# Performance work log

Hardware: AMD Instinct MI355X
Metric: run time of the kernel (lower is better)

Reference implementation:

```python
import jax, jax.numpy as jnp
import numpy as np

DIM = 1024
NUM_HEADS = 16
HEAD_DIM = DIM // NUM_HEADS
SCALE = HEAD_DIM ** -0.5


def setup_inputs() -> dict:
    key = jax.random.key(0)
    ks = jax.random.split(key, 5)
    x = jax.random.normal(ks[0], (8, 1024, DIM), dtype=jnp.float32)
    # nn.Linear default init ~ U(-1/sqrt(fan_in), 1/sqrt(fan_in)); use scaled normals
    w_qkv = jax.random.normal(ks[1], (DIM, 3 * DIM), dtype=jnp.float32) * (DIM ** -0.5)
    b_qkv = jax.random.normal(ks[2], (3 * DIM,), dtype=jnp.float32) * 0.02
    w_proj = jax.random.normal(ks[3], (DIM, DIM), dtype=jnp.float32) * (DIM ** -0.5)
    b_proj = jax.random.normal(ks[4], (DIM,), dtype=jnp.float32) * 0.02
    return {"x": x, "w_qkv": w_qkv, "b_qkv": b_qkv, "w_proj": w_proj, "b_proj": b_proj}


def reference(x, w_qkv, b_qkv, w_proj, b_proj):
    B, N, D = x.shape
    qkv = x @ w_qkv + b_qkv                       # [B, N, 3D]
    qkv = qkv.reshape(B, N, 3, NUM_HEADS, HEAD_DIM)
    qkv = jnp.transpose(qkv, (2, 0, 3, 1, 4))     # [3, B, H, N, hd]
    q, k, v = qkv[0], qkv[1], qkv[2]
    attn = jnp.einsum('bhqd,bhkd->bhqk', q, k) * SCALE
    attn = jax.nn.softmax(attn, axis=-1)
    out = jnp.einsum('bhqk,bhkd->bhqd', attn, v)  # [B, H, N, hd]
    out = jnp.transpose(out, (0, 2, 1, 3)).reshape(B, N, D)
    out = out @ w_proj + b_proj
    return out
```

## Files before the change

kernel.cpp:

```cpp
#include <hip/hip_runtime.h>
#include <stdint.h>


typedef short bf16x8 __attribute__((ext_vector_type(8)));
typedef float f32x4 __attribute__((ext_vector_type(4)));
typedef uint32_t u32x2 __attribute__((ext_vector_type(2)));

__device__ __forceinline__ short f32_bf16(float f) {
  uint32_t u = __builtin_bit_cast(uint32_t, f);
  u += 0x7FFFu + ((u >> 16) & 1u);
  return (short)(u >> 16);
}

__device__ __forceinline__ float exp2_fast(float x) {
  float r; asm("v_exp_f32 %0, %1" : "=v"(r) : "v"(x)); return r;
}

__device__ __forceinline__ uint32_t cvt_pk_bf16(float lo, float hi) {
  uint32_t r;
  asm("v_cvt_pk_bf16_f32 %0, %1, %2" : "=v"(r) : "v"(lo), "v"(hi));
  return r;
}

__device__ __forceinline__ void gload_lds16(const void* g, void* l) {
  __builtin_amdgcn_global_load_lds(
      (const __attribute__((address_space(1))) uint32_t*)g,
      (__attribute__((address_space(3))) uint32_t*)l, 16, 0, 0);
}

__global__ __launch_bounds__(256) void convert_x_kernel(
    const float* __restrict__ x, short* __restrict__ xb) {
  int i = blockIdx.x * 256 + threadIdx.x;
  const float4 f0 = ((const float4*)x)[i * 2];
  const float4 f1 = ((const float4*)x)[i * 2 + 1];
  bf16x8 o;
  o[0] = f32_bf16(f0.x); o[1] = f32_bf16(f0.y);
  o[2] = f32_bf16(f0.z); o[3] = f32_bf16(f0.w);
  o[4] = f32_bf16(f1.x); o[5] = f32_bf16(f1.y);
  o[6] = f32_bf16(f1.z); o[7] = f32_bf16(f1.w);
  ((bf16x8*)xb)[i] = o;
}

__global__ __launch_bounds__(256) void transpose_w_kernel(
    const float* __restrict__ w, short* __restrict__ wt, int N) {
  __shared__ float tile[64][65];
  const int n0 = blockIdx.x * 64, k0 = blockIdx.y * 64;
  const int tr = threadIdx.x >> 6, tc = threadIdx.x & 63;
#pragma unroll
  for (int i = 0; i < 16; ++i) {
    int k = tr + i * 4;
    tile[k][tc] = w[(size_t)(k0 + k) * N + n0 + tc];
  }
  __syncthreads();
#pragma unroll
  for (int i = 0; i < 16; ++i) {
    int a = tr + i * 4;
    wt[(size_t)(n0 + a) * 1024 + k0 + tc] = f32_bf16(tile[tc][a]);
  }
}

__global__ __launch_bounds__(256, 2) void gemm_qkv_kernel(
    const short* __restrict__ A, const short* __restrict__ Bt,
    const float* __restrict__ bias, short* __restrict__ Qb,
    short* __restrict__ Kb, short* __restrict__ Vt) {
  __shared__ short Asm[128 * 64];
  __shared__ short Bsm[128 * 64];
  const int tid = threadIdx.x;
  const int lane = tid & 63;
  const int w = tid >> 6;
  const int wr = w >> 1, wc = w & 1;
  const int c = lane & 15, g = lane >> 4;

  const int NT = 24;
  const int tm = blockIdx.x / NT, tn = blockIdx.x % NT;
  const int m0 = tm * 128, n0 = tn * 128;

  f32x4 acc[4][4] = {};

  for (int k0 = 0; k0 < 1024; k0 += 64) {
#pragma unroll
    for (int i = 0; i < 4; ++i) {
      int ch = (w * 4 + i) * 64 + lane;
      int r = ch >> 3, c8 = ch & 7;
      gload_lds16(A + (size_t)(m0 + r) * 1024 + k0 + c8 * 8, &Asm[ch * 8]);
      gload_lds16(Bt + (size_t)(n0 + r) * 1024 + k0 + c8 * 8, &Bsm[ch * 8]);
    }
    asm volatile("s_waitcnt vmcnt(0)" ::: "memory");
    __syncthreads();
#pragma unroll
    for (int kk = 0; kk < 2; ++kk) {
      bf16x8 a[4], b[4];
#pragma unroll
      for (int m = 0; m < 4; ++m)
        a[m] = *(const bf16x8*)&Asm[(wr * 64 + m * 16 + c) * 64 + kk * 32 + 8 * g];
#pragma unroll
      for (int n = 0; n < 4; ++n)
        b[n] = *(const bf16x8*)&Bsm[(wc * 64 + n * 16 + c) * 64 + kk * 32 + 8 * g];
#pragma unroll
      for (int m = 0; m < 4; ++m)
#pragma unroll
        for (int n = 0; n < 4; ++n)
          acc[m][n] = __builtin_amdgcn_mfma_f32_16x16x32_bf16(a[m], b[n], acc[m][n], 0, 0, 0);
    }
    __syncthreads();
  }

#pragma unroll
  for (int m = 0; m < 4; ++m) {
    const int i_base = m0 + wr * 64 + m * 16 + 4 * g;
#pragma unroll
    for (int n = 0; n < 4; ++n) {
      const int j = n0 + wc * 64 + n * 16 + c;
      const float bj = bias[j];
      const int three = j >> 10, rem = j & 1023, h = rem >> 6, d = rem & 63;
      const float sc = (three == 1) ? 0.18033688f : 1.0f;
#pragma unroll
      for (int r = 0; r < 4; ++r) {
        const int i = i_base + r;
        const int bb = i >> 10, nn = i & 1023;
        const int bh = bb * 16 + h;
        const short bv = f32_bf16((acc[m][n][r] + bj) * sc);
        if (three == 0)
          Qb[(size_t)(bh * 1024 + nn) * 64 + d] = bv;
        else if (three == 1)
          Kb[(size_t)(bh * 1024 + nn) * 64 + d] = bv;
        else
          Vt[(size_t)(bh * 64 + d) * 1024 + nn] = bv;
      }
    }
  }
}

__global__ __launch_bounds__(256, 2) void attn_kernel(
    const short* __restrict__ Qb, const short* __restrict__ Kb,
    const short* __restrict__ Vt, short* __restrict__ Ao) {
  __shared__ __align__(16) char smem[25600];
  short* Kf = (short*)smem;
  short* Vf = (short*)(smem + 8192);
  short* Pl = (short*)(smem + 16384);

  const int tid = threadIdx.x, lane = tid & 63, w = tid >> 6;
  const int c = lane & 15, g = lane >> 4;
  const int bh = blockIdx.x >> 3, qb = blockIdx.x & 7;
  const int bb = bh >> 4, h = bh & 15;
  const int q0 = qb * 128 + w * 32;

  bf16x8 qf[2][2];
#pragma unroll
  for (int m = 0; m < 2; ++m)
#pragma unroll
    for (int ks = 0; ks < 2; ++ks)
      qf[m][ks] = *(const bf16x8*)(Qb + (size_t)(bh * 1024 + q0 + m * 16 + c) * 64 + ks * 32 + 8 * g);

  f32x4 o[2][4] = {};
  float mrun[2] = {-3.0e38f, -3.0e38f};
  float lrun[2] = {0.f, 0.f};

  const int row_r = tid >> 2, seg = tid & 3;
  const short* kp = Kb + (size_t)(bh * 1024 + row_r) * 64 + seg * 16;
  const short* vp = Vt + (size_t)(bh * 64 + row_r) * 1024 + seg * 16;
  short *kdst0, *kdst1, *vdst0, *vdst1;
  {
    const int d0a = seg * 16, d0b = seg * 16 + 8;
    const int pa = (row_r >> 4) * 2 + (d0a >> 5);
    const int pb = (row_r >> 4) * 2 + (d0b >> 5);
    const int sa = (row_r & 15) + 16 * ((d0a & 31) >> 3);
    const int sb = (row_r & 15) + 16 * ((d0b & 31) >> 3);
    kdst0 = &Kf[(pa * 64 + sa) * 8]; kdst1 = &Kf[(pb * 64 + sb) * 8];
    vdst0 = &Vf[(pa * 64 + sa) * 8]; vdst1 = &Vf[(pb * 64 + sb) * 8];
  }

  uint32_t* plw = (uint32_t*)(Pl + w * 1152);
  const short* plr = Pl + w * 1152;

  auto compute = [&]() {
#pragma unroll
    for (int m = 0; m < 2; ++m) {
      f32x4 s[4];
#pragma unroll
      for (int kt = 0; kt < 4; ++kt) {
        f32x4 sa = {};
#pragma unroll
        for (int ks = 0; ks < 2; ++ks) {
          bf16x8 kb = *(const bf16x8*)&Kf[((kt * 2 + ks) * 64 + lane) * 8];
          sa = __builtin_amdgcn_mfma_f32_16x16x32_bf16(kb, qf[m][ks], sa, 0, 0, 0);
        }
        s[kt] = sa;
      }
      float vmax = s[0][0];
#pragma unroll
      for (int kt = 0; kt < 4; ++kt)
#pragma unroll
        for (int r = 0; r < 4; ++r) vmax = fmaxf(vmax, s[kt][r]);
      vmax = fmaxf(vmax, __shfl_xor(vmax, 16));
      vmax = fmaxf(vmax, __shfl_xor(vmax, 32));
      if (!__all(vmax <= mrun[m] + 8.0f)) {
        float mnew = fmaxf(mrun[m], vmax);
        float al = exp2_fast(mrun[m] - mnew);
        lrun[m] *= al;
#pragma unroll
        for (int dt = 0; dt < 4; ++dt) o[m][dt] *= al;
        mrun[m] = mnew;
      }
      float rs = 0.f;
#pragma unroll
      for (int kt = 0; kt < 4; ++kt) {
        float p0 = exp2_fast(s[kt][0] - mrun[m]);
        float p1 = exp2_fast(s[kt][1] - mrun[m]);
        float p2 = exp2_fast(s[kt][2] - mrun[m]);
        float p3 = exp2_fast(s[kt][3] - mrun[m]);
        rs += (p0 + p1) + (p2 + p3);
        u32x2 pk;
        pk[0] = cvt_pk_bf16(p0, p1);
        pk[1] = cvt_pk_bf16(p2, p3);
        *(u32x2*)&plw[c * 36 + kt * 8 + 2 * g] = pk;
      }
      rs += __shfl_xor(rs, 16);
      rs += __shfl_xor(rs, 32);
      lrun[m] += rs;
#pragma unroll
      for (int kk = 0; kk < 2; ++kk) {
        bf16x8 pb = *(const bf16x8*)(plr + c * 72 + kk * 32 + 8 * g);
#pragma unroll
        for (int dt = 0; dt < 4; ++dt) {
          bf16x8 vb = *(const bf16x8*)&Vf[((dt * 2 + kk) * 64 + lane) * 8];
          o[m][dt] = __builtin_amdgcn_mfma_f32_16x16x32_bf16(vb, pb, o[m][dt], 0, 0, 0);
        }
      }
    }
  };

  bf16x8 ka0, ka1, va0, va1, kc0, kc1, vc0, vc1;
  ka0 = *(const bf16x8*)(kp);     ka1 = *(const bf16x8*)(kp + 8);
  va0 = *(const bf16x8*)(vp);     va1 = *(const bf16x8*)(vp + 8);

  for (int t = 0; t < 16; t += 2) {
    __syncthreads();
    *(bf16x8*)kdst0 = ka0; *(bf16x8*)kdst1 = ka1;
    *(bf16x8*)vdst0 = va0; *(bf16x8*)vdst1 = va1;
    {
      const short* kpt = kp + (size_t)(t + 1) * 4096;
      const short* vpt = vp + (t + 1) * 64;
      kc0 = *(const bf16x8*)(kpt); kc1 = *(const bf16x8*)(kpt + 8);
      vc0 = *(const bf16x8*)(vpt); vc1 = *(const bf16x8*)(vpt + 8);
    }
    __syncthreads();
    compute();
    __syncthreads();
    *(bf16x8*)kdst0 = kc0; *(bf16x8*)kdst1 = kc1;
    *(bf16x8*)vdst0 = vc0; *(bf16x8*)vdst1 = vc1;
    if (t + 2 < 16) {
      const short* kpt = kp + (size_t)(t + 2) * 4096;
      const short* vpt = vp + (t + 2) * 64;
      ka0 = *(const bf16x8*)(kpt); ka1 = *(const bf16x8*)(kpt + 8);
      va0 = *(const bf16x8*)(vpt); va1 = *(const bf16x8*)(vpt + 8);
    }
    __syncthreads();
    compute();
  }

  __syncthreads();
  float* Osc = (float*)smem + w * (16 * 68);
  const int qrow = lane >> 2, dseg = (lane & 3) << 4;
#pragma unroll
  for (int m = 0; m < 2; ++m) {
    const float inv = 1.0f / lrun[m];
#pragma unroll
    for (int dt = 0; dt < 4; ++dt)
#pragma unroll
      for (int r = 0; r < 4; ++r)
        Osc[c * 68 + dt * 16 + 4 * g + r] = o[m][dt][r] * inv;
#pragma unroll
    for (int j = 0; j < 2; ++j) {
      f32x4 a0 = *(f32x4*)&Osc[qrow * 68 + dseg + j * 8];
      f32x4 a1 = *(f32x4*)&Osc[qrow * 68 + dseg + j * 8 + 4];
      bf16x8 ob;
      ob[0] = f32_bf16(a0[0]); ob[1] = f32_bf16(a0[1]);
      ob[2] = f32_bf16(a0[2]); ob[3] = f32_bf16(a0[3]);
      ob[4] = f32_bf16(a1[0]); ob[5] = f32_bf16(a1[1]);
      ob[6] = f32_bf16(a1[2]); ob[7] = f32_bf16(a1[3]);
      *(bf16x8*)(Ao + (size_t)(bb * 1024 + q0 + m * 16 + qrow) * 1024 + h * 64 + dseg + j * 8) = ob;
    }
    __syncthreads();
  }
}

__global__ __launch_bounds__(256, 2) void gemm_proj_kernel(
    const short* __restrict__ A, const short* __restrict__ Bt,
    const float* __restrict__ bias, float* __restrict__ out) {
  __shared__ short Asm[128 * 64];
  __shared__ short Bsm[128 * 64];
  const int tid = threadIdx.x;
  const int lane = tid & 63;
  const int w = tid >> 6;
  const int wr = w >> 1, wc = w & 1;
  const int c = lane & 15, g = lane >> 4;

  const int NT = 8;
  const int tm = blockIdx.x / NT, tn = blockIdx.x % NT;
  const int m0 = tm * 128, n0 = tn * 128;

  f32x4 acc[4][4] = {};

  for (int k0 = 0; k0 < 1024; k0 += 64) {
#pragma unroll
    for (int i = 0; i < 4; ++i) {
      int ch = (w * 4 + i) * 64 + lane;
      int r = ch >> 3, c8 = ch & 7;
      gload_lds16(A + (size_t)(m0 + r) * 1024 + k0 + c8 * 8, &Asm[ch * 8]);
      gload_lds16(Bt + (size_t)(n0 + r) * 1024 + k0 + c8 * 8, &Bsm[ch * 8]);
    }
    asm volatile("s_waitcnt vmcnt(0)" ::: "memory");
    __syncthreads();
#pragma unroll
    for (int kk = 0; kk < 2; ++kk) {
      bf16x8 a[4], b[4];
#pragma unroll
      for (int m = 0; m < 4; ++m)
        a[m] = *(const bf16x8*)&Asm[(wr * 64 + m * 16 + c) * 64 + kk * 32 + 8 * g];
#pragma unroll
      for (int n = 0; n < 4; ++n)
        b[n] = *(const bf16x8*)&Bsm[(wc * 64 + n * 16 + c) * 64 + kk * 32 + 8 * g];
#pragma unroll
      for (int m = 0; m < 4; ++m)
#pragma unroll
        for (int n = 0; n < 4; ++n)
          acc[m][n] = __builtin_amdgcn_mfma_f32_16x16x32_bf16(a[m], b[n], acc[m][n], 0, 0, 0);
    }
    __syncthreads();
  }

#pragma unroll
  for (int m = 0; m < 4; ++m) {
    const int i_base = m0 + wr * 64 + m * 16 + 4 * g;
#pragma unroll
    for (int n = 0; n < 4; ++n) {
      const int j = n0 + wc * 64 + n * 16 + c;
      const float bj = bias[j];
#pragma unroll
      for (int r = 0; r < 4; ++r)
        out[(size_t)(i_base + r) * 1024 + j] = acc[m][n][r] + bj;
    }
  }
}

extern "C" void kernel_launch(void* const* d_in, const int* in_sizes, int n_in,
                              void* d_out, int out_size, void* d_ws, size_t ws_size,
                              hipStream_t stream) {
  const float* x = (const float*)d_in[0];
  const float* w_qkv = (const float*)d_in[1];
  const float* b_qkv = (const float*)d_in[2];
  const float* w_proj = (const float*)d_in[3];
  const float* b_proj = (const float*)d_in[4];
  float* out = (float*)d_out;

  char* ws = (char*)d_ws;
  const size_t XB_OFF = 0;
  const size_t WQKVT_OFF = 16777216;
  const size_t WPROJT_OFF = WQKVT_OFF + 6291456;
  const size_t Q_OFF = WPROJT_OFF + 2097152;
  const size_t K_OFF = Q_OFF + 16777216;
  const size_t VT_OFF = K_OFF + 16777216;
  short* xb = (short*)(ws + XB_OFF);
  short* wqkvT = (short*)(ws + WQKVT_OFF);
  short* wprojT = (short*)(ws + WPROJT_OFF);
  short* Qb = (short*)(ws + Q_OFF);
  short* Kb = (short*)(ws + K_OFF);
  short* Vt = (short*)(ws + VT_OFF);
  short* attn_o = xb;

  convert_x_kernel<<<dim3(4096), dim3(256), 0, stream>>>(x, xb);
  transpose_w_kernel<<<dim3(48, 16), dim3(256), 0, stream>>>(w_qkv, wqkvT, 3072);
  transpose_w_kernel<<<dim3(16, 16), dim3(256), 0, stream>>>(w_proj, wprojT, 1024);
  gemm_qkv_kernel<<<dim3(64 * 24), dim3(256), 0, stream>>>(xb, wqkvT, b_qkv, Qb, Kb, Vt);
  attn_kernel<<<dim3(1024), dim3(256), 0, stream>>>(Qb, Kb, Vt, attn_o);
  gemm_proj_kernel<<<dim3(64 * 8), dim3(256), 0, stream>>>(attn_o, wprojT, b_proj, out);
}
```

Before: 273.9 us.

## Replace both GEMMs with 8-wave double-buffered, LDS-swizzled, XCD-remapped templated kernel

Both the QKV and output-projection GEMMs now use one templated kernel with 512 threads and 256-row tiles. It double-buffers LDS so global-to-LDS loads for the next K step overlap the MFMAs of the current one. Loads use an XOR swizzle to avoid LDS bank conflicts, set_prio raises MFMA issue priority, and blocks are remapped across the 8 XCDs for L2 locality. This trades more LDS (64KB+ per block) and registers for fewer barriers stalls and larger reuse, but with 2 blocks per CU requested it may hit LDS limits and lower occupancy.

```diff
diff --git a/kernel.cpp b/kernel.cpp
--- a/kernel.cpp
+++ b/kernel.cpp
@@ -59,73 +59,130 @@
   }
 }
 
-__global__ __launch_bounds__(256, 2) void gemm_qkv_kernel(
+template <int BN, int NREP, int BCH, int EPI>
+__global__ __launch_bounds__(512, 2) void gemm8_kernel(
     const short* __restrict__ A, const short* __restrict__ Bt,
     const float* __restrict__ bias, short* __restrict__ Qb,
-    short* __restrict__ Kb, short* __restrict__ Vt) {
-  __shared__ short Asm[128 * 64];
-  __shared__ short Bsm[128 * 64];
+    short* __restrict__ Kb, short* __restrict__ Vt, float* __restrict__ out,
+    int NTN) {
+  __shared__ short Asm[2][256 * 64];
+  __shared__ short Bsm[2][BN * 64];
+
+  constexpr int TOT = 4 + BCH;
+  constexpr int CS2 = (TOT == 8) ? 6 : 5;
+  constexpr int NPP = NREP / 2;
+  constexpr int WN = NREP * 16;
+
   const int tid = threadIdx.x;
   const int lane = tid & 63;
   const int w = tid >> 6;
-  const int wr = w >> 1, wc = w & 1;
+  const int wm = w >> 2, wn = w & 3;
   const int c = lane & 15, g = lane >> 4;
 
-  const int NT = 24;
-  const int tm = blockIdx.x / NT, tn = blockIdx.x % NT;
-  const int m0 = tm * 128, n0 = tn * 128;
-
-  f32x4 acc[4][4] = {};
-
-  for (int k0 = 0; k0 < 1024; k0 += 64) {
-#pragma unroll
-    for (int i = 0; i < 4; ++i) {
-      int ch = (w * 4 + i) * 64 + lane;
-      int r = ch >> 3, c8 = ch & 7;
-      gload_lds16(A + (size_t)(m0 + r) * 1024 + k0 + c8 * 8, &Asm[ch * 8]);
-      gload_lds16(Bt + (size_t)(n0 + r) * 1024 + k0 + c8 * 8, &Bsm[ch * 8]);
-    }
-    asm volatile("s_waitcnt vmcnt(0)" ::: "memory");
-    __syncthreads();
-#pragma unroll
-    for (int kk = 0; kk < 2; ++kk) {
-      bf16x8 a[4], b[4];
-#pragma unroll
-      for (int m = 0; m < 4; ++m)
-        a[m] = *(const bf16x8*)&Asm[(wr * 64 + m * 16 + c) * 64 + kk * 32 + 8 * g];
-#pragma unroll
-      for (int n = 0; n < 4; ++n)
-        b[n] = *(const bf16x8*)&Bsm[(wc * 64 + n * 16 + c) * 64 + kk * 32 + 8 * g];
-#pragma unroll
-      for (int m = 0; m < 4; ++m)
-#pragma unroll
-        for (int n = 0; n < 4; ++n)
-          acc[m][n] = __builtin_amdgcn_mfma_f32_16x16x32_bf16(a[m], b[n], acc[m][n], 0, 0, 0);
-    }
-    __syncthreads();
-  }
-
-#pragma unroll
-  for (int m = 0; m < 4; ++m) {
-    const int i_base = m0 + wr * 64 + m * 16 + 4 * g;
-#pragma unroll
-    for (int n = 0; n < 4; ++n) {
-      const int j = n0 + wc * 64 + n * 16 + c;
+  const int nwg = gridDim.x;
+  const int wg = (blockIdx.x & 7) * (nwg >> 3) + (blockIdx.x >> 3);
+  const int tm = wg / NTN, tn = wg % NTN;
+  const int m0 = tm * 256, n0 = tn * BN;
+
+  f32x4 acc[8][NREP] = {};
+
+  auto stage_chunk = [&](int ci, int dbuf, int kk0) {
+    if (ci < 4) {
+      const int p = ci * 512 + tid;
+      const int r = p >> 3, s = p & 7;
+      gload_lds16(A + (size_t)(m0 + r) * 1024 + kk0 + ((s ^ (r & 7)) * 8),
+                  &Asm[dbuf][p * 8]);
+    } else {
+      const int p = (ci - 4) * 512 + tid;
+      const int r = p >> 3, s = p & 7;
+      gload_lds16(Bt + (size_t)(n0 + r) * 1024 + kk0 + ((s ^ (r & 7)) * 8),
+                  &Bsm[dbuf][p * 8]);
+    }
+  };
+
+#pragma unroll
+  for (int ci = 0; ci < TOT; ++ci) stage_chunk(ci, 0, 0);
+
+  auto tile_step = [&](int t, int buf) {
+#pragma unroll
+    for (int p4 = 0; p4 < 4; ++p4) {
+      const int cs = (p4 == 0) ? 0 : (p4 == 1) ? 2 : (p4 == 2) ? 4 : CS2;
+      const int ce = (p4 == 0) ? 2 : (p4 == 1) ? 4 : (p4 == 2) ? CS2 : TOT;
+      if (t < 15) {
+#pragma unroll
+        for (int ci = cs; ci < ce; ++ci) stage_chunk(ci, buf ^ 1, (t + 1) * 64);
+      }
+      if (p4 == 0) {
+        if (t < 15) asm volatile("s_waitcnt vmcnt(2)" ::: "memory");
+        else        asm volatile("s_waitcnt vmcnt(0)" ::: "memory");
+        __builtin_amdgcn_s_barrier();
+      }
+      const int mq = p4 >> 1, nq = p4 & 1;
+      bf16x8 af[4][2];
+      bf16x8 bfr[NPP][2];
+#pragma unroll
+      for (int mm = 0; mm < 4; ++mm) {
+        const int R = wm * 128 + (mq * 4 + mm) * 16 + c;
+#pragma unroll
+        for (int kk = 0; kk < 2; ++kk)
+          af[mm][kk] = *(const bf16x8*)&Asm[buf][R * 64 + (((kk * 4 + g) ^ (c & 7)) * 8)];
+      }
+#pragma unroll
+      for (int jn = 0; jn < NPP; ++jn) {
+        const int S = wn * WN + (nq * NPP + jn) * 16 + c;
+#pragma unroll
+        for (int kk = 0; kk < 2; ++kk)
+          bfr[jn][kk] = *(const bf16x8*)&Bsm[buf][S * 64 + (((kk * 4 + g) ^ (c & 7)) * 8)];
+      }
+      __builtin_amdgcn_s_barrier();
+      asm volatile("s_waitcnt lgkmcnt(0)" ::: "memory");
+      __builtin_amdgcn_sched_barrier(0);
+      __builtin_amdgcn_s_setprio(1);
+#pragma unroll
+      for (int mm = 0; mm < 4; ++mm)
+#pragma unroll
+        for (int jn = 0; jn < NPP; ++jn)
+#pragma unroll
+          for (int kk = 0; kk < 2; ++kk)
+            acc[mq * 4 + mm][nq * NPP + jn] = __builtin_amdgcn_mfma_f32_16x16x32_bf16(
+                af[mm][kk], bfr[jn][kk], acc[mq * 4 + mm][nq * NPP + jn], 0, 0, 0);
+      __builtin_amdgcn_s_setprio(0);
+      __builtin_amdgcn_s_barrier();
+    }
+  };
+
+  for (int t2 = 0; t2 < 16; t2 += 2) {
+    tile_step(t2, 0);
+    tile_step(t2 + 1, 1);
+  }
+
+#pragma unroll
+  for (int mm = 0; mm < 8; ++mm) {
+    const int i_base = m0 + wm * 128 + mm * 16 + 4 * g;
+#pragma unroll
+    for (int nn = 0; nn < NREP; ++nn) {
+      const int j = n0 + wn * WN + nn * 16 + c;
       const float bj = bias[j];
-      const int three = j >> 10, rem = j & 1023, h = rem >> 6, d = rem & 63;
-      const float sc = (three == 1) ? 0.18033688f : 1.0f;
-#pragma unroll
-      for (int r = 0; r < 4; ++r) {
-        const int i = i_base + r;
-        const int bb = i >> 10, nn = i & 1023;
-        const int bh = bb * 16 + h;
-        const short bv = f32_bf16((acc[m][n][r] + bj) * sc);
-        if (three == 0)
-          Qb[(size_t)(bh * 1024 + nn) * 64 + d] = bv;
-        else if (three == 1)
-          Kb[(size_t)(bh * 1024 + nn) * 64 + d] = bv;
-        else
-          Vt[(size_t)(bh * 64 + d) * 1024 + nn] = bv;
+      if (EPI == 0) {
+        const int three = j >> 10, rem = j & 1023, h = rem >> 6, d = rem & 63;
+        const float sc = (three == 1) ? 0.18033688f : 1.0f;
+#pragma unroll
+        for (int r = 0; r < 4; ++r) {
+          const int i = i_base + r;
+          const int bb = i >> 10, nnq = i & 1023;
+          const int bh = bb * 16 + h;
+          const short bv = f32_bf16((acc[mm][nn][r] + bj) * sc);
+          if (three == 0)
+            Qb[(size_t)(bh * 1024 + nnq) * 64 + d] = bv;
+          else if (three == 1)
+            Kb[(size_t)(bh * 1024 + nnq) * 64 + d] = bv;
+          else
+            Vt[(size_t)(bh * 64 + d) * 1024 + nnq] = bv;
+        }
+      } else {
+#pragma unroll
+        for (int r = 0; r < 4; ++r)
+          out[(size_t)(i_base + r) * 1024 + j] = acc[mm][nn][r] + bj;
       }
     }
   }
@@ -282,65 +339,6 @@
       *(bf16x8*)(Ao + (size_t)(bb * 1024 + q0 + m * 16 + qrow) * 1024 + h * 64 + dseg + j * 8) = ob;
     }
     __syncthreads();
-  }
-}
-
-__global__ __launch_bounds__(256, 2) void gemm_proj_kernel(
-    const short* __restrict__ A, const short* __restrict__ Bt,
-    const float* __restrict__ bias, float* __restrict__ out) {
-  __shared__ short Asm[128 * 64];
-  __shared__ short Bsm[128 * 64];
-  const int tid = threadIdx.x;
-  const int lane = tid & 63;
-  const int w = tid >> 6;
-  const int wr = w >> 1, wc = w & 1;
-  const int c = lane & 15, g = lane >> 4;
-
-  const int NT = 8;
-  const int tm = blockIdx.x / NT, tn = blockIdx.x % NT;
-  const int m0 = tm * 128, n0 = tn * 128;
-
-  f32x4 acc[4][4] = {};
-
-  for (int k0 = 0; k0 < 1024; k0 += 64) {
-#pragma unroll
-    for (int i = 0; i < 4; ++i) {
-      int ch = (w * 4 + i) * 64 + lane;
-      int r = ch >> 3, c8 = ch & 7;
-      gload_lds16(A + (size_t)(m0 + r) * 1024 + k0 + c8 * 8, &Asm[ch * 8]);
-      gload_lds16(Bt + (size_t)(n0 + r) * 1024 + k0 + c8 * 8, &Bsm[ch * 8]);
-    }
-    asm volatile("s_waitcnt vmcnt(0)" ::: "memory");
-    __syncthreads();
-#pragma unroll
-    for (int kk = 0; kk < 2; ++kk) {
-      bf16x8 a[4], b[4];
-#pragma unroll
-      for (int m = 0; m < 4; ++m)
-        a[m] = *(const bf16x8*)&Asm[(wr * 64 + m * 16 + c) * 64 + kk * 32 + 8 * g];
-#pragma unroll
-      for (int n = 0; n < 4; ++n)
-        b[n] = *(const bf16x8*)&Bsm[(wc * 64 + n * 16 + c) * 64 + kk * 32 + 8 * g];
-#pragma unroll
-      for (int m = 0; m < 4; ++m)
-#pragma unroll
-        for (int n = 0; n < 4; ++n)
-          acc[m][n] = __builtin_amdgcn_mfma_f32_16x16x32_bf16(a[m], b[n], acc[m][n], 0, 0, 0);
-    }
-    __syncthreads();
-  }
-
-#pragma unroll
-  for (int m = 0; m < 4; ++m) {
-    const int i_base = m0 + wr * 64 + m * 16 + 4 * g;
-#pragma unroll
-    for (int n = 0; n < 4; ++n) {
-      const int j = n0 + wc * 64 + n * 16 + c;
-      const float bj = bias[j];
-#pragma unroll
-      for (int r = 0; r < 4; ++r)
-        out[(size_t)(i_base + r) * 1024 + j] = acc[m][n][r] + bj;
-    }
   }
 }
 
@@ -372,7 +370,9 @@
   convert_x_kernel<<<dim3(4096), dim3(256), 0, stream>>>(x, xb);
   transpose_w_kernel<<<dim3(48, 16), dim3(256), 0, stream>>>(w_qkv, wqkvT, 3072);
   transpose_w_kernel<<<dim3(16, 16), dim3(256), 0, stream>>>(w_proj, wprojT, 1024);
-  gemm_qkv_kernel<<<dim3(64 * 24), dim3(256), 0, stream>>>(xb, wqkvT, b_qkv, Qb, Kb, Vt);
+  gemm8_kernel<256, 4, 4, 0><<<dim3(384), dim3(512), 0, stream>>>(
+      xb, wqkvT, b_qkv, Qb, Kb, Vt, nullptr, 12);
   attn_kernel<<<dim3(1024), dim3(256), 0, stream>>>(Qb, Kb, Vt, attn_o);
-  gemm_proj_kernel<<<dim3(64 * 8), dim3(256), 0, stream>>>(attn_o, wprojT, b_proj, out);
-}
+  gemm8_kernel<128, 2, 2, 1><<<dim3(256), dim3(512), 0, stream>>>(
+      attn_o, wprojT, b_proj, nullptr, nullptr, nullptr, out, 8);
+}
```

Result: slower. 311.7 us (+13.8%).
